# Performance work log

Hardware: AMD Instinct MI355X
Metric: run time of the kernel (lower is better)

## Reference

```python
import jax, jax.numpy as jnp
import numpy as np

N = 16384
DIMS = [3, 128, 128, 128, 128, 128, 128, 128, 128, 2]
N_LAYERS = len(DIMS) - 1  # 9 linear layers


def setup_inputs() -> dict:
    key = jax.random.key(0)
    ks = jax.random.split(key, 2 * N_LAYERS + 3)
    d = {}
    for i in range(N_LAYERS):
        fan_in = DIMS[i]
        d[f"W{i}"] = (jax.random.normal(ks[2 * i], (DIMS[i + 1], DIMS[i]), dtype=jnp.float32)
                      / jnp.sqrt(jnp.float32(fan_in)))
        d[f"b{i}"] = jnp.zeros((DIMS[i + 1],), dtype=jnp.float32)
    d["x"] = jax.random.normal(ks[-3], (N, 1), dtype=jnp.float32)
    d["y"] = jax.random.normal(ks[-2], (N, 1), dtype=jnp.float32)
    d["t"] = jax.random.uniform(ks[-1], (N, 1), dtype=jnp.float32)
    d["lambda_1"] = jnp.zeros((1,), dtype=jnp.float32)
    d["lambda_2"] = jnp.zeros((1,), dtype=jnp.float32)
    return d


def reference(x, y, t, lambda_1, lambda_2,
              W0, b0, W1, b1, W2, b2, W3, b3, W4, b4,
              W5, b5, W6, b6, W7, b7, W8, b8):
    Ws = [W0, W1, W2, W3, W4, W5, W6, W7, W8]
    bs = [b0, b1, b2, b3, b4, b5, b6, b7, b8]

    def net(z):  # z: (3,) -> (2,) = (psi, p)
        h = z
        for W, b in zip(Ws[:-1], bs[:-1]):
            h = jnp.tanh(W @ h + b)
        return Ws[-1] @ h + bs[-1]

    psi_fn = lambda z: net(z)[0]
    p_fn = lambda z: net(z)[1]

    l1 = lambda_1[0]
    l2 = lambda_2[0]

    def per_point(z):
        # z = (x, y, t); index 0->x, 1->y, 2->t
        g = jax.grad(psi_fn)(z)                       # (3,)  psi_x, psi_y, psi_t
        H = jax.jacfwd(jax.grad(psi_fn))(z)           # (3,3) psi_ij
        T = jax.jacfwd(jax.jacfwd(jax.grad(psi_fn)))(z)  # (3,3,3) psi_ijk
        p = p_fn(z)
        gp = jax.grad(p_fn)(z)
        u = g[1]          # psi_y
        v = -g[0]         # -psi_x
        u_x, u_y, u_t = H[1, 0], H[1, 1], H[1, 2]
        v_x, v_y, v_t = -H[0, 0], -H[0, 1], -H[0, 2]
        u_xx, u_yy = T[1, 0, 0], T[1, 1, 1]
        v_xx, v_yy = -T[0, 0, 0], -T[0, 1, 1]
        p_x, p_y = gp[0], gp[1]
        f_u = u_t + l1 * (u * u_x + v * u_y) + p_x - l2 * (u_xx + u_yy)
        f_v = v_t + l1 * (u * v_x + v * v_y) + p_y - l2 * (v_xx + v_yy)
        return u, v, p, f_u, f_v

    Z = jnp.concatenate([x, y, t], axis=1)  # [N, 3]
    u, v, p, f_u, f_v = jax.vmap(per_point)(Z)
    return (u[:, None], v[:, None], p[:, None], f_u[:, None], f_v[:, None])
```

## Files before the change

### kernel.cpp

```cpp
#include <hip/hip_runtime.h>
#include <stdint.h>

#define NPTS 16384

typedef __attribute__((ext_vector_type(8)))  __bf16   bf16x8;
typedef __attribute__((ext_vector_type(16))) float    f32x16;
typedef __attribute__((ext_vector_type(4)))  float    f32x4;
typedef __attribute__((ext_vector_type(4)))  uint32_t u32x4;

struct PrepArgs {
    const float* W[7];
    u32x4* dst;
    const float* l1; const float* l2;
    int run_on_zero;
};

struct Args {
    const float* W0; const float* b0;
    const float* bias[8];
    const float* W8; const float* b8;
    const float* xs; const float* ys; const float* ts;
    const float* l1; const float* l2;
    const u32x4* wpk;
    const u32x4* wpk16;
    float* out;
};

__device__ __forceinline__ uint32_t b16rne(float x) {
    uint32_t u = __float_as_uint(x);
    return (u + 0x7FFFu + ((u >> 16) & 1u)) >> 16;
}
__device__ __forceinline__ float fromb16(uint32_t h) { return __uint_as_float(h << 16); }

__device__ __forceinline__ void packPair(float a, float b, uint32_t& hw, uint32_t& lw) {
    uint32_t ha = b16rne(a), hb = b16rne(b);
    float la = a - fromb16(ha), lb = b - fromb16(hb);
    hw = ha | (hb << 16);
    lw = b16rne(la) | (b16rne(lb) << 16);
}

__device__ __forceinline__ uint32_t cvtpk_bf16(float a, float b) {
    uint32_t r;
    asm("v_cvt_pk_bf16_f32 %0, %1, %2" : "=v"(r) : "v"(a), "v"(b));
    return r;
}

__device__ __forceinline__ f32x16 mfma32(bf16x8 a, bf16x8 b, f32x16 c) {
    return __builtin_amdgcn_mfma_f32_32x32x16_bf16(a, b, c, 0, 0, 0);
}
__device__ __forceinline__ f32x4 mfma16(bf16x8 a, bf16x8 b, f32x4 c) {
    return __builtin_amdgcn_mfma_f32_16x16x32_bf16(a, b, c, 0, 0, 0);
}

__device__ __forceinline__ float fast_tanh(float x) {
    float e = __expf(2.0f * x);
    return 1.0f - __fdividef(2.0f, e + 1.0f);
}

__device__ __forceinline__ void tanh_jet(float u[13]) {
    float s    = fast_tanh(u[0]);
    float sp   = 1.f - s * s;
    float spp  = -2.f * s * sp;
    float sppp = -2.f * (sp * sp + s * spp);
    float u1 = u[1], u2 = u[2], u3 = u[3];
    float u4 = u[4], u5 = u[5], u6 = u[6];
    u[0] = s;
    u[1] = sp * u1;
    u[2] = sp * u2;
    u[3] = sp * u3;
    u[9]  = sppp * u1 * u1 * u1 + 3.f * spp * u1 * u4 + sp * u[9];
    u[10] = sppp * u1 * u1 * u2 + spp * (u4 * u2 + 2.f * u5 * u1) + sp * u[10];
    u[11] = sppp * u1 * u2 * u2 + spp * (u6 * u1 + 2.f * u5 * u2) + sp * u[11];
    u[12] = sppp * u2 * u2 * u2 + 3.f * spp * u2 * u6 + sp * u[12];
    u[4] = spp * u1 * u1 + sp * u4;
    u[5] = spp * u1 * u2 + sp * u5;
    u[6] = spp * u2 * u2 + sp * u6;
    u[7] = spp * u1 * u3 + sp * u[7];
    u[8] = spp * u2 * u3 + sp * u[8];
}

__device__ __forceinline__ void tanh_jet6(float u[6]) {
    float s   = fast_tanh(u[0]);
    float sp  = 1.f - s * s;
    float spp = -2.f * s * sp;
    float u1 = u[1], u2 = u[2], u3 = u[3];
    u[0] = s;
    u[4] = spp * u1 * u3 + sp * u[4];
    u[5] = spp * u2 * u3 + sp * u[5];
    u[1] = sp * u1;
    u[2] = sp * u2;
    u[3] = sp * u3;
}

__global__ __launch_bounds__(256)
void pack_w_kernel(PrepArgs a) {
    bool z = (a.l1[0] == 0.f && a.l2[0] == 0.f);
    if (z != (bool)a.run_on_zero) return;
    int idx = blockIdx.x * 256 + threadIdx.x;
    int L  = idx >> 11;
    int kb = (idx >> 7) & 15;
    int n  = idx & 127;
    const float* w = a.W[L] + n * 128 + kb * 8;
    float4 f0 = *(const float4*)w;
    float4 f1 = *(const float4*)(w + 4);
    uint32_t h0, h1, h2, h3, l0, l1, l2, l3;
    packPair(f0.x, f0.y, h0, l0);
    packPair(f0.z, f0.w, h1, l1);
    packPair(f1.x, f1.y, h2, l2);
    packPair(f1.z, f1.w, h3, l3);
    a.dst[((L * 2 + 0) * 16 + kb) * 128 + n] = u32x4{h0, h1, h2, h3};
    a.dst[((L * 2 + 1) * 16 + kb) * 128 + n] = u32x4{l0, l1, l2, l3};
}

__global__ __launch_bounds__(256)
void pack_w16_kernel(PrepArgs a) {
    bool z = (a.l1[0] == 0.f && a.l2[0] == 0.f);
    if (z != (bool)a.run_on_zero) return;
    int idx = blockIdx.x * 256 + threadIdx.x;
    int L = idx >> 11;
    int s = (idx >> 9) & 3;
    int g = (idx >> 7) & 3;
    int n = idx & 127;
    const float* w = a.W[L] + n * 128 + s * 32 + g * 8;
    float4 f0 = *(const float4*)w;
    float4 f1 = *(const float4*)(w + 4);
    uint32_t h0, h1, h2, h3, l0, l1, l2, l3;
    packPair(f0.x, f0.y, h0, l0);
    packPair(f0.z, f0.w, h1, l1);
    packPair(f1.x, f1.y, h2, l2);
    packPair(f1.z, f1.w, h3, l3);
    a.dst[((L * 2 + 0) * 16 + s * 4 + g) * 128 + n] = u32x4{h0, h1, h2, h3};
    a.dst[((L * 2 + 1) * 16 + s * 4 + g) * 128 + n] = u32x4{l0, l1, l2, l3};
}

__global__ __launch_bounds__(256, 3)
void pinn_red2s_kernel(Args args)
{
    if (args.l1[0] != 0.f || args.l2[0] != 0.f) return;

    __shared__ ushort Ahi[2][48 * 128];
    __shared__ ushort Alo[2][48 * 128];
    float* Part = (float*)&Ahi[0][0];

    const int tid   = threadIdx.x;
    const int lane  = tid & 63;
    const int wid   = tid >> 6;
    const int l15   = lane & 15;
    const int g     = lane >> 4;
    const int n0    = wid * 32 + l15;
    const int pbase = blockIdx.x * 16;

    auto put_pair = [&](ushort* Ah, ushort* Al, float dA, float dB, int rowA, int n) {
        const int rowB = rowA + 1;
        const int aA = rowA * 128 + ((((n >> 3) ^ (rowA & 15)) << 3) | (n & 7));
        const int aB = rowB * 128 + ((((n >> 3) ^ (rowB & 15)) << 3) | (n & 7));
        uint32_t hp = cvtpk_bf16(dA, dB);
        float hA = __uint_as_float(hp << 16);
        float hB = __uint_as_float(hp & 0xFFFF0000u);
        uint32_t lp = cvtpk_bf16(dA - hA, dB - hB);
        Ah[aA] = (ushort)hp;  Ah[aB] = (ushort)(hp >> 16);
        Al[aA] = (ushort)lp;  Al[aB] = (ushort)(lp >> 16);
    };
    auto store_jet6 = [&](int set, const float d[6], int e, int n) {
        ushort* Ah = Ahi[set];
        ushort* Al = Alo[set];
        #pragma unroll
        for (int cp = 0; cp < 3; ++cp) {
            const int rowA = 16 * cp + 4 * g + 2 * e;
            put_pair(Ah, Al, d[2 * cp], d[2 * cp + 1], rowA, n);
        }
    };

    #pragma unroll
    for (int ct = 0; ct < 2; ++ct) {
        const int n = n0 + 16 * ct;
        float w0 = args.W0[n * 3], w1 = args.W0[n * 3 + 1], w2 = args.W0[n * 3 + 2];
        float bb = args.b0[n];
        #pragma unroll
        for (int set = 0; set < 2; ++set) {
            #pragma unroll
            for (int e = 0; e < 2; ++e) {
                const int pt = pbase + 8 * set + 2 * g + e;
                float x = args.xs[pt], y = args.ys[pt], tt = args.ts[pt];
                float d[6];
                d[0] = w0 * x + w1 * y + w2 * tt + bb;
                d[1] = w0; d[2] = w1; d[3] = w2;
                d[4] = 0.f; d[5] = 0.f;
                tanh_jet6(d);
                store_jet6(set, d, e, n);
            }
        }
    }
    __syncthreads();

    for (int L = 1; L <= 7; ++L) {
        const u32x4* whi = args.wpk16 + (size_t)(L - 1) * 4096;
        const u32x4* wlo = whi + 2048;
        f32x4 a000{}, a001{}, a002{}, a010{}, a011{}, a012{};
        f32x4 a100{}, a101{}, a102{}, a110{}, a111{}, a112{};

        #pragma unroll
        for (int s = 0; s < 4; ++s) {
            const int gb   = s * 4 + g;
            const int koff = (gb ^ l15) << 3;
            const bf16x8 bh0 = __builtin_bit_cast(bf16x8, whi[gb * 128 + n0]);
            const bf16x8 bh1 = __builtin_bit_cast(bf16x8, whi[gb * 128 + n0 + 16]);
            const bf16x8 bl0 = __builtin_bit_cast(bf16x8, wlo[gb * 128 + n0]);
            const bf16x8 bl1 = __builtin_bit_cast(bf16x8, wlo[gb * 128 + n0 + 16]);

            auto gemm_set = [&](const ushort* Ah, const ushort* Al,
                                f32x4& c00, f32x4& c01, f32x4& c02,
                                f32x4& c10, f32x4& c11, f32x4& c12) {
                bf16x8 ah0 = __builtin_bit_cast(bf16x8, *(const u32x4*)&Ah[(     l15) * 128 + koff]);
                bf16x8 ah1 = __builtin_bit_cast(bf16x8, *(const u32x4*)&Ah[(16 + l15) * 128 + koff]);
                bf16x8 ah2 = __builtin_bit_cast(bf16x8, *(const u32x4*)&Ah[(32 + l15) * 128 + koff]);
                bf16x8 al0 = __builtin_bit_cast(bf16x8, *(const u32x4*)&Al[(     l15) * 128 + koff]);
                bf16x8 al1 = __builtin_bit_cast(bf16x8, *(const u32x4*)&Al[(16 + l15) * 128 + koff]);
                bf16x8 al2 = __builtin_bit_cast(bf16x8, *(const u32x4*)&Al[(32 + l15) * 128 + koff]);
                c00 = mfma16(ah0, bh0, c00);
                c01 = mfma16(ah1, bh0, c01);
                c02 = mfma16(ah2, bh0, c02);
                c10 = mfma16(ah0, bh1, c10);
                c11 = mfma16(ah1, bh1, c11);
                c12 = mfma16(ah2, bh1, c12);
                c00 = mfma16(al0, bh0, c00);
                c01 = mfma16(al1, bh0, c01);
                c02 = mfma16(al2, bh0, c02);
                c10 = mfma16(al0, bh1, c10);
                c11 = mfma16(al1, bh1, c11);
                c12 = mfma16(al2, bh1, c12);
                c00 = mfma16(ah0, bl0, c00);
                c01 = mfma16(ah1, bl0, c01);
                c02 = mfma16(ah2, bl0, c02);
                c10 = mfma16(ah0, bl1, c10);
                c11 = mfma16(ah1, bl1, c11);
                c12 = mfma16(ah2, bl1, c12);
            };
            gemm_set(Ahi[0], Alo[0], a000, a001, a002, a010, a011, a012);
            gemm_set(Ahi[1], Alo[1], a100, a101, a102, a110, a111, a112);
        }

        __syncthreads();

        auto getd = [&](int set, int ct, int e, float d[6]) {
            const f32x4 r0 = (set == 0) ? ((ct == 0) ? a000 : a010) : ((ct == 0) ? a100 : a110);
            const f32x4 r1 = (set == 0) ? ((ct == 0) ? a001 : a011) : ((ct == 0) ? a101 : a111);
            const f32x4 r2 = (set == 0) ? ((ct == 0) ? a002 : a012) : ((ct == 0) ? a102 : a112);
            d[0] = r0[2 * e]; d[1] = r0[1 + 2 * e];
            d[2] = r1[2 * e]; d[3] = r1[1 + 2 * e];
            d[4] = r2[2 * e]; d[5] = r2[1 + 2 * e];
        };

        if (L < 7) {
            #pragma unroll
            for (int ct = 0; ct < 2; ++ct) {
                const int n = n0 + 16 * ct;
                const float bL = args.bias[L][n];
                #pragma unroll
                for (int set = 0; set < 2; ++set) {
                    #pragma unroll
                    for (int e = 0; e < 2; ++e) {
                        float d[6];
                        getd(set, ct, e, d);
                        d[0] += bL;
                        tanh_jet6(d);
                        store_jet6(set, d, e, n);
                    }
                }
            }
            __syncthreads();
        } else {
            #pragma unroll
            for (int set = 0; set < 2; ++set) {
                #pragma unroll
                for (int e = 0; e < 2; ++e) {
                    float rp[9];
                    #pragma unroll
                    for (int v = 0; v < 9; ++v) rp[v] = 0.f;
                    #pragma unroll
                    for (int ct = 0; ct < 2; ++ct) {
                        const int n = n0 + 16 * ct;
                        const float bL = args.bias[7][n];
                        const float wp = args.W8[n], wq = args.W8[128 + n];
                        float d[6];
                        getd(set, ct, e, d);
                        d[0] += bL;
                        tanh_jet6(d);
                        #pragma unroll
                        for (int c = 0; c < 6; ++c) rp[c] += wp * d[c];
                        rp[6] += wq * d[0]; rp[7] += wq * d[1]; rp[8] += wq * d[2];
                    }
                    #pragma unroll
                    for (int v = 0; v < 9; ++v) {
                        float sv = rp[v];
                        sv += __shfl_xor(sv, 8); sv += __shfl_xor(sv, 4);
                        sv += __shfl_xor(sv, 2); sv += __shfl_xor(sv, 1);
                        rp[v] = sv;
                    }
                    if (l15 == 0) {
                        #pragma unroll
                        for (int v = 0; v < 9; ++v)
                            Part[(((set * 4 + wid) * 4 + g) * 2 + e) * 9 + v] = rp[v];
                    }
                }
            }
        }
    }

    __syncthreads();

    if (tid < 16) {
        const int set = tid >> 3, rem = tid & 7;
        const int gg = rem >> 1, e = rem & 1;
        float s[9];
        #pragma unroll
        for (int v = 0; v < 9; ++v) {
            float acc = 0.f;
            #pragma unroll
            for (int w = 0; w < 4; ++w)
                acc += Part[(((set * 4 + w) * 4 + gg) * 2 + e) * 9 + v];
            s[v] = acc;
        }

        float u   = s[2];
        float v   = -s[1];
        float pv  = s[6] + args.b8[1];
        float f_u = s[5] + s[7];
        float f_v = -s[4] + s[8];
        const int pt = pbase + 8 * set + rem;
        float* out = args.out;
        out[0 * NPTS + pt] = u;
        out[1 * NPTS + pt] = v;
        out[2 * NPTS + pt] = pv;
        out[3 * NPTS + pt] = f_u;
        out[4 * NPTS + pt] = f_v;
    }
}

__global__ __launch_bounds__(256, 2)
void pinn_mfma6_kernel(Args args)
{
    if (args.l1[0] == 0.f && args.l2[0] == 0.f) return;

    __shared__ ushort Ahi[128 * 128];
    __shared__ ushort Alo[128 * 128];
    __shared__ float  Part[4][2][4][16];

    const int tid   = threadIdx.x;
    const int lane  = tid & 63;
    const int wid   = tid >> 6;
    const int ln31  = lane & 31;
    const int kh    = lane >> 5;
    const int n     = wid * 32 + ln31;
    const int pbase = blockIdx.x * 8;

    auto store_jet = [&](const float d[13], int j) {
        const int rb = 32 * j + 4 * kh;
        #pragma unroll
        for (int cp = 0; cp < 6; ++cp) {
            const int cA = 2 * cp, cB = cA + 1;
            const int rowA = rb + 8 * (cA >> 2) + (cA & 3);
            const int rowB = rb + 8 * (cB >> 2) + (cB & 3);
            const int aA = rowA * 128 + ((((n >> 3) ^ (rowA & 15)) << 3) | (n & 7));
            const int aB = rowB * 128 + ((((n >> 3) ^ (rowB & 15)) << 3) | (n & 7));
            uint32_t hp = cvtpk_bf16(d[cA], d[cB]);
            float hA = __uint_as_float(hp << 16);
            float hB = __uint_as_float(hp & 0xFFFF0000u);
            uint32_t lp = cvtpk_bf16(d[cA] - hA, d[cB] - hB);
            Ahi[aA] = (ushort)hp; Ahi[aB] = (ushort)(hp >> 16);
            Alo[aA] = (ushort)lp; Alo[aB] = (ushort)(lp >> 16);
        }
        {
            const int row = rb + 24;
            const int a12 = row * 128 + ((((n >> 3) ^ (row & 15)) << 3) | (n & 7));
            uint32_t hp = cvtpk_bf16(d[12], 0.f);
            float h = __uint_as_float(hp << 16);
            uint32_t lp = cvtpk_bf16(d[12] - h, 0.f);
            Ahi[a12] = (ushort)hp;
            Alo[a12] = (ushort)lp;
        }
    };

    {
        float w0 = args.W0[n * 3], w1 = args.W0[n * 3 + 1], w2 = args.W0[n * 3 + 2];
        float bb = args.b0[n];
        #pragma unroll
        for (int j = 0; j < 4; ++j) {
            const int p = j + 4 * kh;
            float x = args.xs[pbase + p], y = args.ys[pbase + p], t = args.ts[pbase + p];
            float d[13];
            #pragma unroll
            for (int c = 4; c < 13; ++c) d[c] = 0.f;
            d[0] = w0 * x + w1 * y + w2 * t + bb;
            d[1] = w0; d[2] = w1; d[3] = w2;
            tanh_jet(d);
            store_jet(d, j);
        }
        #pragma unroll
        for (int i = 0; i < 12; ++i) {
            int idx  = tid + 256 * i;
            int pl   = (idx >= 1536) ? 1 : 0;
            int rem  = idx - 1536 * pl;
            int rowi = rem >> 6;
            int w    = rem & 63;
            int t4   = rowi / 6, s = rowi - 6 * t4;
            int row  = 32 * t4 + 24 + 4 * (s / 3) + 1 + (s % 3);
            uint32_t* P = pl ? (uint32_t*)Alo : (uint32_t*)Ahi;
            P[row * 64 + w] = 0;
        }
    }
    __syncthreads();

    for (int L = 1; L <= 7; ++L) {
        const u32x4* whi = args.wpk + (size_t)(L - 1) * 4096;
        const u32x4* wlo = whi + 2048;
        f32x16 acc0{}, acc1{}, acc2{}, acc3{};

        #pragma unroll
        for (int ks = 0; ks < 8; ++ks) {
            const int kb = ks * 2 + kh;
            const u32x4 rbh = whi[kb * 128 + n];
            const u32x4 rbl = wlo[kb * 128 + n];

            const int koff = (kb ^ (ln31 & 15)) << 3;
            const int e0 = (ln31      ) * 128 + koff;
            const int e1 = (ln31 + 32 ) * 128 + koff;
            const int e2 = (ln31 + 64 ) * 128 + koff;
            const int e3 = (ln31 + 96 ) * 128 + koff;
            bf16x8 ah0 = __builtin_bit_cast(bf16x8, *(const u32x4*)&Ahi[e0]);
            bf16x8 ah1 = __builtin_bit_cast(bf16x8, *(const u32x4*)&Ahi[e1]);
            bf16x8 ah2 = __builtin_bit_cast(bf16x8, *(const u32x4*)&Ahi[e2]);
            bf16x8 ah3 = __builtin_bit_cast(bf16x8, *(const u32x4*)&Ahi[e3]);
            bf16x8 al0 = __builtin_bit_cast(bf16x8, *(const u32x4*)&Alo[e0]);
            bf16x8 al1 = __builtin_bit_cast(bf16x8, *(const u32x4*)&Alo[e1]);
            bf16x8 al2 = __builtin_bit_cast(bf16x8, *(const u32x4*)&Alo[e2]);
            bf16x8 al3 = __builtin_bit_cast(bf16x8, *(const u32x4*)&Alo[e3]);
            bf16x8 bh  = __builtin_bit_cast(bf16x8, rbh);
            bf16x8 bl  = __builtin_bit_cast(bf16x8, rbl);

            acc0 = mfma32(ah0, bh, acc0);
            acc1 = mfma32(ah1, bh, acc1);
            acc2 = mfma32(ah2, bh, acc2);
            acc3 = mfma32(ah3, bh, acc3);
            acc0 = mfma32(al0, bh, acc0);
            acc1 = mfma32(al1, bh, acc1);
            acc2 = mfma32(al2, bh, acc2);
            acc3 = mfma32(al3, bh, acc3);
            acc0 = mfma32(ah0, bl, acc0);
            acc1 = mfma32(ah1, bl, acc1);
            acc2 = mfma32(ah2, bl, acc2);
            acc3 = mfma32(ah3, bl, acc3);
        }

        __syncthreads();

        const float bL = args.bias[L][n];

        if (L < 7) {
            #pragma unroll
            for (int j = 0; j < 4; ++j) {
                float d[13];
                #pragma unroll
                for (int c = 0; c < 13; ++c)
                    d[c] = (j == 0) ? acc0[c] : (j == 1) ? acc1[c] : (j == 2) ? acc2[c] : acc3[c];
                d[0] += bL;
                tanh_jet(d);
                store_jet(d, j);
            }
            __syncthreads();
        } else {
            const float wp = args.W8[n], wq = args.W8[128 + n];
            #pragma unroll
            for (int j = 0; j < 4; ++j) {
                float d[13];
                #pragma unroll
                for (int c = 0; c < 13; ++c)
                    d[c] = (j == 0) ? acc0[c] : (j == 1) ? acc1[c] : (j == 2) ? acc2[c] : acc3[c];
                d[0] += bL;
                tanh_jet(d);
                float rp[16];
                #pragma unroll
                for (int c = 0; c < 13; ++c) rp[c] = wp * d[c];
                rp[13] = wq * d[0]; rp[14] = wq * d[1]; rp[15] = wq * d[2];
                #pragma unroll
                for (int v = 0; v < 16; ++v) {
                    float s = rp[v];
                    s += __shfl_xor(s, 16); s += __shfl_xor(s, 8);
                    s += __shfl_xor(s, 4);  s += __shfl_xor(s, 2);
                    s += __shfl_xor(s, 1);
                    rp[v] = s;
                }
                if (ln31 == 0) {
                    #pragma unroll
                    for (int v = 0; v < 16; ++v) Part[wid][kh][j][v] = rp[v];
                }
            }
        }
    }

    __syncthreads();

    if (tid < 8) {
        const int p = tid, khp = p >> 2, jp = p & 3;
        float s[16];
        #pragma unroll
        for (int v = 0; v < 16; ++v)
            s[v] = Part[0][khp][jp][v] + Part[1][khp][jp][v]
                 + Part[2][khp][jp][v] + Part[3][khp][jp][v];

        float l1 = args.l1[0], l2 = args.l2[0];
        float u    = s[2];
        float v    = -s[1];
        float pv   = s[13] + args.b8[1];
        float u_t  = s[8];
        float v_t  = -s[7];
        float u_x  = s[5];
        float u_y  = s[6];
        float v_x  = -s[4];
        float v_y  = -s[5];
        float u_xx = s[10];
        float u_yy = s[12];
        float v_xx = -s[9];
        float v_yy = -s[11];
        float p_x = s[14], p_y = s[15];
        float f_u = u_t + l1 * (u * u_x + v * u_y) + p_x - l2 * (u_xx + u_yy);
        float f_v = v_t + l1 * (u * v_x + v * v_y) + p_y - l2 * (v_xx + v_yy);
        const int pt = pbase + p;
        float* out = args.out;
        out[0 * NPTS + pt] = u;
        out[1 * NPTS + pt] = v;
        out[2 * NPTS + pt] = pv;
        out[3 * NPTS + pt] = f_u;
        out[4 * NPTS + pt] = f_v;
    }
}

extern "C" void kernel_launch(void* const* d_in, const int* in_sizes, int n_in,
                              void* d_out, int out_size, void* d_ws, size_t ws_size,
                              hipStream_t stream) {
    const float* l1p = (const float*)d_in[21];
    const float* l2p = (const float*)d_in[22];

    u32x4* wpk16 = (u32x4*)d_ws;
    u32x4* wpkOld = (u32x4*)((char*)d_ws + 448 * 1024);

    PrepArgs pa16;
    for (int i = 0; i < 7; ++i) pa16.W[i] = (const float*)d_in[2 * (i + 1)];
    pa16.dst = wpk16; pa16.l1 = l1p; pa16.l2 = l2p; pa16.run_on_zero = 1;
    pack_w16_kernel<<<56, 256, 0, stream>>>(pa16);

    PrepArgs paOld = pa16;
    paOld.dst = wpkOld; paOld.run_on_zero = 0;
    pack_w_kernel<<<56, 256, 0, stream>>>(paOld);

    Args a;
    a.W0 = (const float*)d_in[0];
    a.b0 = (const float*)d_in[1];
    a.bias[0] = nullptr;
    for (int L = 1; L <= 7; ++L) a.bias[L] = (const float*)d_in[2 * L + 1];
    a.W8 = (const float*)d_in[16];
    a.b8 = (const float*)d_in[17];
    a.xs = (const float*)d_in[18];
    a.ys = (const float*)d_in[19];
    a.ts = (const float*)d_in[20];
    a.l1 = l1p;
    a.l2 = l2p;
    a.wpk = wpkOld;
    a.wpk16 = wpk16;
    a.out = (float*)d_out;

    pinn_red2s_kernel<<<NPTS / 16, 256, 0, stream>>>(a);
    pinn_mfma6_kernel<<<NPTS / 8, 256, 0, stream>>>(a);
}
```

Measured before the change: 83.02 us.

## Software-pipeline two point sets so MFMA GEMM overlaps tanh jet epilogue

The layer loop is restructured so the two point sets are staggered by half a layer. While one set's GEMM runs on the matrix cores, the other set's tanh-jet activation and LDS store runs on the vector units, between the same barriers. The aim is to hide the transcendental and VALU epilogue behind the MFMA work, which used to run serially after both GEMMs. The cost is more live accumulator registers across phases, which may raise register pressure and affect the 3-blocks-per-CU target.

```diff
diff --git a/kernel.cpp b/kernel.cpp
--- a/kernel.cpp
+++ b/kernel.cpp
@@ -134,7 +134,7 @@
 }
 
 __global__ __launch_bounds__(256, 3)
-void pinn_red2s_kernel(Args args)
+void pinn_red2p_kernel(Args args)
 {
     if (args.l1[0] != 0.f || args.l2[0] != 0.f) return;
 
@@ -171,6 +171,112 @@
         }
     };
 
+    f32x4 a000{}, a001{}, a002{}, a010{}, a011{}, a012{};
+    f32x4 a100{}, a101{}, a102{}, a110{}, a111{}, a112{};
+
+    auto run_gemm = [&](const ushort* Ah, const ushort* Al,
+                        const u32x4* whi, const u32x4* wlo,
+                        f32x4& c00, f32x4& c01, f32x4& c02,
+                        f32x4& c10, f32x4& c11, f32x4& c12) {
+        c00 = f32x4{}; c01 = f32x4{}; c02 = f32x4{};
+        c10 = f32x4{}; c11 = f32x4{}; c12 = f32x4{};
+        #pragma unroll
+        for (int s = 0; s < 4; ++s) {
+            const int gb   = s * 4 + g;
+            const int koff = (gb ^ l15) << 3;
+            const bf16x8 bh0 = __builtin_bit_cast(bf16x8, whi[gb * 128 + n0]);
+            const bf16x8 bh1 = __builtin_bit_cast(bf16x8, whi[gb * 128 + n0 + 16]);
+            const bf16x8 bl0 = __builtin_bit_cast(bf16x8, wlo[gb * 128 + n0]);
+            const bf16x8 bl1 = __builtin_bit_cast(bf16x8, wlo[gb * 128 + n0 + 16]);
+            bf16x8 ah0 = __builtin_bit_cast(bf16x8, *(const u32x4*)&Ah[(     l15) * 128 + koff]);
+            bf16x8 ah1 = __builtin_bit_cast(bf16x8, *(const u32x4*)&Ah[(16 + l15) * 128 + koff]);
+            bf16x8 ah2 = __builtin_bit_cast(bf16x8, *(const u32x4*)&Ah[(32 + l15) * 128 + koff]);
+            bf16x8 al0 = __builtin_bit_cast(bf16x8, *(const u32x4*)&Al[(     l15) * 128 + koff]);
+            bf16x8 al1 = __builtin_bit_cast(bf16x8, *(const u32x4*)&Al[(16 + l15) * 128 + koff]);
+            bf16x8 al2 = __builtin_bit_cast(bf16x8, *(const u32x4*)&Al[(32 + l15) * 128 + koff]);
+            c00 = mfma16(ah0, bh0, c00);
+            c01 = mfma16(ah1, bh0, c01);
+            c02 = mfma16(ah2, bh0, c02);
+            c10 = mfma16(ah0, bh1, c10);
+            c11 = mfma16(ah1, bh1, c11);
+            c12 = mfma16(ah2, bh1, c12);
+            c00 = mfma16(al0, bh0, c00);
+            c01 = mfma16(al1, bh0, c01);
+            c02 = mfma16(al2, bh0, c02);
+            c10 = mfma16(al0, bh1, c10);
+            c11 = mfma16(al1, bh1, c11);
+            c12 = mfma16(al2, bh1, c12);
+            c00 = mfma16(ah0, bl0, c00);
+            c01 = mfma16(ah1, bl0, c01);
+            c02 = mfma16(ah2, bl0, c02);
+            c10 = mfma16(ah0, bl1, c10);
+            c11 = mfma16(ah1, bl1, c11);
+            c12 = mfma16(ah2, bl1, c12);
+        }
+    };
+
+    auto getd = [&](int e, const f32x4& r0, const f32x4& r1, const f32x4& r2, float d[6]) {
+        d[0] = r0[2 * e]; d[1] = r0[1 + 2 * e];
+        d[2] = r1[2 * e]; d[3] = r1[1 + 2 * e];
+        d[4] = r2[2 * e]; d[5] = r2[1 + 2 * e];
+    };
+
+    auto tanh_store = [&](int set, int L,
+                          f32x4& c00, f32x4& c01, f32x4& c02,
+                          f32x4& c10, f32x4& c11, f32x4& c12) {
+        #pragma unroll
+        for (int ct = 0; ct < 2; ++ct) {
+            const int n = n0 + 16 * ct;
+            const float bL = args.bias[L][n];
+            #pragma unroll
+            for (int e = 0; e < 2; ++e) {
+                float d[6];
+                if (ct == 0) getd(e, c00, c01, c02, d);
+                else         getd(e, c10, c11, c12, d);
+                d[0] += bL;
+                tanh_jet6(d);
+                store_jet6(set, d, e, n);
+            }
+        }
+    };
+
+    auto tanh_reduce = [&](int set,
+                           f32x4& c00, f32x4& c01, f32x4& c02,
+                           f32x4& c10, f32x4& c11, f32x4& c12) {
+        #pragma unroll
+        for (int e = 0; e < 2; ++e) {
+            float rp[9];
+            #pragma unroll
+            for (int v = 0; v < 9; ++v) rp[v] = 0.f;
+            #pragma unroll
+            for (int ct = 0; ct < 2; ++ct) {
+                const int n = n0 + 16 * ct;
+                const float bL = args.bias[7][n];
+                const float wp = args.W8[n], wq = args.W8[128 + n];
+                float d[6];
+                if (ct == 0) getd(e, c00, c01, c02, d);
+                else         getd(e, c10, c11, c12, d);
+                d[0] += bL;
+                tanh_jet6(d);
+                #pragma unroll
+                for (int c = 0; c < 6; ++c) rp[c] += wp * d[c];
+                rp[6] += wq * d[0]; rp[7] += wq * d[1]; rp[8] += wq * d[2];
+            }
+            #pragma unroll
+            for (int v = 0; v < 9; ++v) {
+                float sv = rp[v];
+                sv += __shfl_xor(sv, 8); sv += __shfl_xor(sv, 4);
+                sv += __shfl_xor(sv, 2); sv += __shfl_xor(sv, 1);
+                rp[v] = sv;
+            }
+            if (l15 == 0) {
+                #pragma unroll
+                for (int v = 0; v < 9; ++v)
+                    Part[(((set * 4 + wid) * 4 + g) * 2 + e) * 9 + v] = rp[v];
+            }
+        }
+    };
+
     #pragma unroll
     for (int ct = 0; ct < 2; ++ct) {
         const int n = n0 + 16 * ct;
@@ -193,121 +299,32 @@
     }
     __syncthreads();
 
+    run_gemm(Ahi[0], Alo[0], args.wpk16, args.wpk16 + 2048,
+             a000, a001, a002, a010, a011, a012);
+    __syncthreads();
+
     for (int L = 1; L <= 7; ++L) {
-        const u32x4* whi = args.wpk16 + (size_t)(L - 1) * 4096;
-        const u32x4* wlo = whi + 2048;
-        f32x4 a000{}, a001{}, a002{}, a010{}, a011{}, a012{};
-        f32x4 a100{}, a101{}, a102{}, a110{}, a111{}, a112{};
-
-        #pragma unroll
-        for (int s = 0; s < 4; ++s) {
-            const int gb   = s * 4 + g;
-            const int koff = (gb ^ l15) << 3;
-            const bf16x8 bh0 = __builtin_bit_cast(bf16x8, whi[gb * 128 + n0]);
-            const bf16x8 bh1 = __builtin_bit_cast(bf16x8, whi[gb * 128 + n0 + 16]);
-            const bf16x8 bl0 = __builtin_bit_cast(bf16x8, wlo[gb * 128 + n0]);
-            const bf16x8 bl1 = __builtin_bit_cast(bf16x8, wlo[gb * 128 + n0 + 16]);
-
-            auto gemm_set = [&](const ushort* Ah, const ushort* Al,
-                                f32x4& c00, f32x4& c01, f32x4& c02,
-                                f32x4& c10, f32x4& c11, f32x4& c12) {
-                bf16x8 ah0 = __builtin_bit_cast(bf16x8, *(const u32x4*)&Ah[(     l15) * 128 + koff]);
-                bf16x8 ah1 = __builtin_bit_cast(bf16x8, *(const u32x4*)&Ah[(16 + l15) * 128 + koff]);
-                bf16x8 ah2 = __builtin_bit_cast(bf16x8, *(const u32x4*)&Ah[(32 + l15) * 128 + koff]);
-                bf16x8 al0 = __builtin_bit_cast(bf16x8, *(const u32x4*)&Al[(     l15) * 128 + koff]);
-                bf16x8 al1 = __builtin_bit_cast(bf16x8, *(const u32x4*)&Al[(16 + l15) * 128 + koff]);
-                bf16x8 al2 = __builtin_bit_cast(bf16x8, *(const u32x4*)&Al[(32 + l15) * 128 + koff]);
-                c00 = mfma16(ah0, bh0, c00);
-                c01 = mfma16(ah1, bh0, c01);
-                c02 = mfma16(ah2, bh0, c02);
-                c10 = mfma16(ah0, bh1, c10);
-                c11 = mfma16(ah1, bh1, c11);
-                c12 = mfma16(ah2, bh1, c12);
-                c00 = mfma16(al0, bh0, c00);
-                c01 = mfma16(al1, bh0, c01);
-                c02 = mfma16(al2, bh0, c02);
-                c10 = mfma16(al0, bh1, c10);
-                c11 = mfma16(al1, bh1, c11);
-                c12 = mfma16(al2, bh1, c12);
-                c00 = mfma16(ah0, bl0, c00);
-                c01 = mfma16(ah1, bl0, c01);
-                c02 = mfma16(ah2, bl0, c02);
-                c10 = mfma16(ah0, bl1, c10);
-                c11 = mfma16(ah1, bl1, c11);
-                c12 = mfma16(ah2, bl1, c12);
-            };
-            gemm_set(Ahi[0], Alo[0], a000, a001, a002, a010, a011, a012);
-            gemm_set(Ahi[1], Alo[1], a100, a101, a102, a110, a111, a112);
-        }
-
+        const u32x4* whiL = args.wpk16 + (size_t)(L - 1) * 4096;
+
+        run_gemm(Ahi[1], Alo[1], whiL, whiL + 2048,
+                 a100, a101, a102, a110, a111, a112);
+        if (L < 7)
+            tanh_store(0, L, a000, a001, a002, a010, a011, a012);
+        else
+            tanh_reduce(0, a000, a001, a002, a010, a011, a012);
         __syncthreads();
 
-        auto getd = [&](int set, int ct, int e, float d[6]) {
-            const f32x4 r0 = (set == 0) ? ((ct == 0) ? a000 : a010) : ((ct == 0) ? a100 : a110);
-            const f32x4 r1 = (set == 0) ? ((ct == 0) ? a001 : a011) : ((ct == 0) ? a101 : a111);
-            const f32x4 r2 = (set == 0) ? ((ct == 0) ? a002 : a012) : ((ct == 0) ? a102 : a112);
-            d[0] = r0[2 * e]; d[1] = r0[1 + 2 * e];
-            d[2] = r1[2 * e]; d[3] = r1[1 + 2 * e];
-            d[4] = r2[2 * e]; d[5] = r2[1 + 2 * e];
-        };
-
         if (L < 7) {
-            #pragma unroll
-            for (int ct = 0; ct < 2; ++ct) {
-                const int n = n0 + 16 * ct;
-                const float bL = args.bias[L][n];
-                #pragma unroll
-                for (int set = 0; set < 2; ++set) {
-                    #pragma unroll
-                    for (int e = 0; e < 2; ++e) {
-                        float d[6];
-                        getd(set, ct, e, d);
-                        d[0] += bL;
-                        tanh_jet6(d);
-                        store_jet6(set, d, e, n);
-                    }
-                }
-            }
+            const u32x4* whiN = args.wpk16 + (size_t)L * 4096;
+            run_gemm(Ahi[0], Alo[0], whiN, whiN + 2048,
+                     a000, a001, a002, a010, a011, a012);
+            tanh_store(1, L, a100, a101, a102, a110, a111, a112);
             __syncthreads();
         } else {
-            #pragma unroll
-            for (int set = 0; set < 2; ++set) {
-                #pragma unroll
-                for (int e = 0; e < 2; ++e) {
-                    float rp[9];
-                    #pragma unroll
-                    for (int v = 0; v < 9; ++v) rp[v] = 0.f;
-                    #pragma unroll
-                    for (int ct = 0; ct < 2; ++ct) {
-                        const int n = n0 + 16 * ct;
-                        const float bL = args.bias[7][n];
-                        const float wp = args.W8[n], wq = args.W8[128 + n];
-                        float d[6];
-                        getd(set, ct, e, d);
-                        d[0] += bL;
-                        tanh_jet6(d);
-                        #pragma unroll
-                        for (int c = 0; c < 6; ++c) rp[c] += wp * d[c];
-                        rp[6] += wq * d[0]; rp[7] += wq * d[1]; rp[8] += wq * d[2];
-                    }
-                    #pragma unroll
-                    for (int v = 0; v < 9; ++v) {
-                        float sv = rp[v];
-                        sv += __shfl_xor(sv, 8); sv += __shfl_xor(sv, 4);
-                        sv += __shfl_xor(sv, 2); sv += __shfl_xor(sv, 1);
-                        rp[v] = sv;
-                    }
-                    if (l15 == 0) {
-                        #pragma unroll
-                        for (int v = 0; v < 9; ++v)
-                            Part[(((set * 4 + wid) * 4 + g) * 2 + e) * 9 + v] = rp[v];
-                    }
-                }
-            }
+            tanh_reduce(1, a100, a101, a102, a110, a111, a112);
+            __syncthreads();
         }
     }
-
-    __syncthreads();
 
     if (tid < 16) {
         const int set = tid >> 3, rem = tid & 7;
@@ -569,6 +586,6 @@
     a.wpk16 = wpk16;
     a.out = (float*)d_out;
 
-    pinn_red2s_kernel<<<NPTS / 16, 256, 0, stream>>>(a);
+    pinn_red2p_kernel<<<NPTS / 16, 256, 0, stream>>>(a);
     pinn_mfma6_kernel<<<NPTS / 8, 256, 0, stream>>>(a);
 }
```

Result: slower. 110.2 us (+32.8%).
